# Optimization experiments

Measured on AMD Instinct MI355X. Metric: run time of the kernel, lower is better.

Reference implementation:

```python
import jax, jax.numpy as jnp
import numpy as np

DIM = 128
NUM_HEADS = 2
HEAD_DIM = DIM // NUM_HEADS
SCALE = HEAD_DIM ** -0.5
SR = 4
EPS_LN = 1e-5


def token2map(x, idx_token, H, W, H_init, W_init):
    """Scatter tokens x[B,N,Cc] into a [B,Cc,H,W] map via the init grid.
    Matches the sparse-COO branch of the torch token2map (N_init < N*H*W).
    """
    B, N, Cc = x.shape
    N_init = H_init * W_init
    # nearest-neighbor index of each init-grid cell in the HxW map
    rows = (jnp.arange(H_init) * H) // H_init          # floor(i * H / H_init)
    cols = (jnp.arange(W_init) * W) // W_init
    idx_hw = (rows[:, None] * W + cols[None, :]).reshape(-1)      # [N_init]
    flat = (idx_hw[None, :] + jnp.arange(B)[:, None] * (H * W)).reshape(-1)  # [B*N_init]
    # per-pixel count (A @ ones) + 1e-6, as in torch
    count = jax.ops.segment_sum(jnp.ones((B * N_init,), jnp.float32), flat,
                                num_segments=B * H * W) + 1e-6    # [B*H*W]
    gathered = jnp.take_along_axis(x, idx_token[..., None], axis=1)  # [B,N_init,Cc]
    out = jax.ops.segment_sum(gathered.reshape(B * N_init, Cc), flat,
                              num_segments=B * H * W)
    out = out / count[:, None]
    return out.reshape(B, H, W, Cc).transpose(0, 3, 1, 2)  # [B,Cc,H,W]


def setup_inputs() -> dict:
    key = jax.random.key(0)
    ks = jax.random.split(key, 12)
    B, Nq, Nkv, C = 8, 12544, 12544, DIM
    H, W, H_init, W_init = 112, 112, 224, 224
    inp = {
        'q_x': jax.random.normal(ks[0], (B, Nq, C), jnp.float32),
        'kv_x': jax.random.normal(ks[1], (B, Nkv, C), jnp.float32),
        'token_score': jax.random.normal(ks[2], (B, Nkv, 1), jnp.float32),
        'idx_token': jax.random.randint(ks[3], (B, H_init * W_init), 0, Nkv),
        'H': H, 'W': W, 'H_init': H_init, 'W_init': W_init,
        # learned params (qkv_bias=False)
        'q_w': jax.random.normal(ks[4], (C, C), jnp.float32) * 0.02,
        'kv_w': jax.random.normal(ks[5], (C, 2 * C), jnp.float32) * 0.02,
        'proj_w': jax.random.normal(ks[6], (C, C), jnp.float32) * 0.02,
        'proj_b': jnp.zeros((C,), jnp.float32),
        'sr_w': jax.random.normal(ks[7], (C, C, SR, SR), jnp.float32) * np.sqrt(2.0 / (SR * SR * C)),
        'sr_b': jnp.zeros((C,), jnp.float32),
        'norm_g': jnp.ones((C,), jnp.float32),
        'norm_b': jnp.zeros((C,), jnp.float32),
    }
    return inp


def reference(q_x, kv_x, token_score, q_w, kv_w, proj_w, proj_b, sr_w, sr_b,
              norm_g, norm_b, idx_token, H, W, H_init, W_init):
    B, Nq, C = q_x.shape
    # q projection -> [B, h, Nq, d]
    q = (q_x @ q_w).reshape(B, Nq, NUM_HEADS, HEAD_DIM).transpose(0, 2, 1, 3)

    # sr_ratio > 1 path: scatter kv tokens (with conf channel) to q's map
    tmp = jnp.concatenate([kv_x, token_score], axis=-1)          # [B,Nkv,C+1]
    tmp_map = token2map(tmp, idx_token, H, W, H_init, W_init)    # [B,C+1,H,W]
    kv_map = tmp_map[:, :C]                                      # [B,C,H,W]
    conf_map = tmp_map[:, C:]                                    # [B,1,H,W]

    # spatial reduction conv (kernel=stride=SR) + LayerNorm
    kv_r = jax.lax.conv_general_dilated(
        kv_map, sr_w, window_strides=(SR, SR), padding='VALID',
        dimension_numbers=('NCHW', 'OIHW', 'NCHW')) + sr_b[None, :, None, None]
    h, w = kv_r.shape[2], kv_r.shape[3]
    Ns = h * w
    kv_t = kv_r.reshape(B, C, Ns).transpose(0, 2, 1)             # [B,Ns,C]
    mu = jnp.mean(kv_t, axis=-1, keepdims=True)
    var = jnp.mean(jnp.square(kv_t - mu), axis=-1, keepdims=True)
    kv_t = (kv_t - mu) / jnp.sqrt(var + EPS_LN) * norm_g + norm_b

    # avg-pool conf to the reduced grid
    conf = conf_map.reshape(B, 1, h, SR, w, SR).mean(axis=(3, 5)).reshape(B, Ns)

    # kv projection -> k,v [B,h,Ns,d]
    kv_p = (kv_t @ kv_w).reshape(B, Ns, 2, NUM_HEADS, HEAD_DIM).transpose(2, 0, 3, 1, 4)
    k, v = kv_p[0], kv_p[1]

    attn = jnp.einsum('bhqd,bhkd->bhqk', q * SCALE, k) + conf[:, None, None, :]
    attn = jax.nn.softmax(attn, axis=-1)
    out = jnp.einsum('bhqk,bhkd->bhqd', attn, v).transpose(0, 2, 1, 3).reshape(B, Nq, C)
    return out @ proj_w + proj_b
```

## Files before the change

### kernel.cpp

```cpp
#include <hip/hip_runtime.h>
#include <hip/hip_bf16.h>


#define NBATCH 8
#define NQTOK  12544
#define NSP    832
#define LOG2E  1.4426950408889634f
#define QSCALE (0.125f * LOG2E)

typedef __attribute__((ext_vector_type(8))) short bf8;
typedef __attribute__((ext_vector_type(4))) float f4;
typedef __attribute__((ext_vector_type(4))) unsigned short u16x4;
typedef __attribute__((ext_vector_type(2))) unsigned int u32x2;

#define MFMA16(a, b, c) __builtin_amdgcn_mfma_f32_16x16x32_bf16((a), (b), (c), 0, 0, 0)

#if __has_builtin(__builtin_amdgcn_exp2f)
#define EXP2(x) __builtin_amdgcn_exp2f(x)
#else
#define EXP2(x) exp2f(x)
#endif

__device__ __forceinline__ unsigned short f2b(float x) {
  union { float f; unsigned u; } v; v.f = x;
  unsigned r = v.u + 0x7FFFu + ((v.u >> 16) & 1u);
  return (unsigned short)(r >> 16);
}

__device__ __forceinline__ unsigned pk2(float lo, float hi) {
  float2 t; t.x = lo; t.y = hi;
  __hip_bfloat162 bb = __float22bfloat162_rn(t);
  union { __hip_bfloat162 b; unsigned u; } v; v.b = bb;
  return v.u;
}

__device__ __forceinline__ bf8 rows2frag(const unsigned W0[2], const unsigned W1[2]) {
  u32x2 r0 = __builtin_amdgcn_permlane32_swap(W0[0], W1[0], false, false);
  u32x2 t02 = __builtin_amdgcn_permlane16_swap(r0.x, r0.y, false, false);
  u32x2 r1 = __builtin_amdgcn_permlane32_swap(W0[1], W1[1], false, false);
  u32x2 t13 = __builtin_amdgcn_permlane16_swap(r1.x, r1.y, false, false);
  union { unsigned u[4]; bf8 v; } pa;
  pa.u[0] = t02.x; pa.u[1] = t13.x; pa.u[2] = t02.y; pa.u[3] = t13.y;
  return pa.v;
}

__device__ __forceinline__ bf8 ldfrag(const unsigned short* t, int stride, int rbase, int kbase) {
  int lane = threadIdx.x & 63;
  return *(const bf8*)(t + (rbase + (lane & 15)) * stride + kbase + ((lane >> 4) << 3));
}

__global__ void k_token2map(const float* __restrict__ kv_x, const float* __restrict__ tsc,
                            const int* __restrict__ idxt,
                            unsigned short* __restrict__ kv_map, float* __restrict__ conf_map,
                            const float* __restrict__ qw, const float* __restrict__ kvw,
                            const float* __restrict__ pw, const float* __restrict__ srw,
                            unsigned short* __restrict__ qwt, unsigned short* __restrict__ kvwt,
                            unsigned short* __restrict__ pwt, unsigned short* __restrict__ srwt,
                            unsigned* __restrict__ kb, unsigned* __restrict__ vb,
                            float* __restrict__ conf) {
  int tid = threadIdx.x;
  int bid = blockIdx.x;
  if (bid >= 12544) {
    int t = (bid - 12544) * 256 + tid;
    int nt = 256 * 256;
    for (int i = t; i < 128 * 128; i += nt) {
      int k = i >> 7, n = i & 127;
      qwt[n * 128 + k] = f2b(qw[k * 128 + n] * QSCALE);
      pwt[n * 128 + k] = f2b(pw[k * 128 + n]);
    }
    for (int i = t; i < 128 * 256; i += nt) {
      int k = i >> 8, j = i & 255;
      kvwt[j * 128 + k] = f2b(kvw[k * 256 + j]);
    }
    for (int i = t; i < 128 * 2048; i += nt) {
      int o = i >> 11, kk = i & 2047;
      int p = kk >> 7, c = kk & 127;
      srwt[o * 2048 + kk] = f2b(srw[o * 2048 + c * 16 + p]);
    }
    const int nu = NBATCH * 2 * NSP * 64 / 2;
    for (int i = t; i < nu; i += nt) { kb[i] = 0u; vb[i] = 0u; }
    for (int i = t; i < NBATCH * NSP; i += nt) conf[i] = -1e30f;
    return;
  }
  int b = bid & 7, pos = bid >> 3;
  int hw = pos * 8 + (tid >> 5);
  int cell = b * 12544 + hw;
  int c0 = (tid & 31) << 2;
  int h = hw / 112, w = hw - h * 112;
  const int* it = idxt + b * 50176;
  int t0 = it[(2 * h) * 224 + 2 * w];
  int t1 = it[(2 * h) * 224 + 2 * w + 1];
  int t2 = it[(2 * h + 1) * 224 + 2 * w];
  int t3 = it[(2 * h + 1) * 224 + 2 * w + 1];
  const float* base = kv_x + (long)b * 12544 * 128 + c0;
  const float recip = 1.0f / (4.0f + 1e-6f);
  float4 a0 = *(const float4*)(base + (long)t0 * 128);
  float4 a1 = *(const float4*)(base + (long)t1 * 128);
  float4 a2 = *(const float4*)(base + (long)t2 * 128);
  float4 a3 = *(const float4*)(base + (long)t3 * 128);
  u16x4 o;
  o[0] = f2b((a0.x + a1.x + a2.x + a3.x) * recip);
  o[1] = f2b((a0.y + a1.y + a2.y + a3.y) * recip);
  o[2] = f2b((a0.z + a1.z + a2.z + a3.z) * recip);
  o[3] = f2b((a0.w + a1.w + a2.w + a3.w) * recip);
  *(u16x4*)(kv_map + (long)cell * 128 + c0) = o;
  if ((tid & 31) == 0) {
    const float* ts = tsc + b * 12544;
    conf_map[cell] = (ts[t0] + ts[t1] + ts[t2] + ts[t3]) * recip;
  }
}

__launch_bounds__(256)
__global__ void k_conv_ln_kv(const unsigned short* __restrict__ kv_map,
                             const unsigned short* __restrict__ srwt,
                             const float* __restrict__ srb, const float* __restrict__ ng,
                             const float* __restrict__ nb,
                             const unsigned short* __restrict__ kvwt,
                             unsigned short* __restrict__ kbuf,
                             unsigned short* __restrict__ vbuf,
                             const float* __restrict__ conf_map, float* __restrict__ conf) {
  __shared__ unsigned short At[64 * 136];
  __shared__ unsigned short Bt[128 * 136];
  const int tid = threadIdx.x;
  const int lane = tid & 63, w = tid >> 6;
  const int l15 = lane & 15, g = lane >> 4;
  const int r0 = blockIdx.x * 64;
  if (tid < 64) {
    int pos = r0 + tid;
    int bq = pos / 784, p2 = pos - bq * 784;
    int oh = p2 / 28, ow = p2 - oh * 28;
    float s = 0.f;
#pragma unroll
    for (int kh = 0; kh < 4; kh++)
#pragma unroll
      for (int kw = 0; kw < 4; kw++)
        s += conf_map[bq * 12544 + (4 * oh + kh) * 112 + 4 * ow + kw];
    conf[bq * NSP + p2] = s * (LOG2E / 16.0f);
  }
  const f4 fz = {0.f, 0.f, 0.f, 0.f};
  f4 acc[8];
#pragma unroll
  for (int i = 0; i < 8; i++) acc[i] = fz;

  for (int p = 0; p < 16; p++) {
#pragma unroll
    for (int j = 0; j < 4; j++) {
      int id = tid + 256 * j;
      int row = id >> 4, c0 = (id & 15) << 3;
      int rr = r0 + row;
      int bb = rr / 784, pos = rr - bb * 784;
      int oh = pos / 28, ow = pos - oh * 28;
      long src = ((long)(bb * 12544 + (4 * oh + (p >> 2)) * 112 + 4 * ow + (p & 3))) * 128 + c0;
      *(uint4*)(At + row * 136 + c0) = *(const uint4*)(kv_map + src);
    }
#pragma unroll
    for (int j = 0; j < 8; j++) {
      int id = tid + 256 * j;
      int row = id >> 4, c0 = (id & 15) << 3;
      *(uint4*)(Bt + row * 136 + c0) = *(const uint4*)(srwt + row * 2048 + p * 128 + c0);
    }
    __syncthreads();
#pragma unroll
    for (int ks = 0; ks < 4; ks++) {
      bf8 a = ldfrag(At, 136, 16 * w, 32 * ks);
#pragma unroll
      for (int nf = 0; nf < 8; nf++) {
        bf8 bb = ldfrag(Bt, 136, 16 * nf, 32 * ks);
        acc[nf] = MFMA16(a, bb, acc[nf]);
      }
    }
    __syncthreads();
  }
  float sum_[4] = {0.f, 0.f, 0.f, 0.f}, sq_[4] = {0.f, 0.f, 0.f, 0.f};
#pragma unroll
  for (int nf = 0; nf < 8; nf++) {
    float bias = srb[16 * nf + l15];
#pragma unroll
    for (int reg = 0; reg < 4; reg++) {
      float v = acc[nf][reg] + bias;
      acc[nf][reg] = v;
      sum_[reg] += v;
      sq_[reg] += v * v;
    }
  }
#pragma unroll
  for (int msk = 1; msk < 16; msk <<= 1)
#pragma unroll
    for (int reg = 0; reg < 4; reg++) {
      sum_[reg] += __shfl_xor(sum_[reg], msk, 64);
      sq_[reg] += __shfl_xor(sq_[reg], msk, 64);
    }
#pragma unroll
  for (int nf = 0; nf < 8; nf++) {
    float gc = ng[16 * nf + l15], bc = nb[16 * nf + l15];
#pragma unroll
    for (int reg = 0; reg < 4; reg++) {
      float mean = sum_[reg] * (1.0f / 128.0f);
      float var = sq_[reg] * (1.0f / 128.0f) - mean * mean;
      float v = (acc[nf][reg] - mean) * rsqrtf(var + 1e-5f) * gc + bc;
      At[(16 * w + 4 * g + reg) * 136 + 16 * nf + l15] = f2b(v);
    }
  }
  __syncthreads();
  f4 acc2[16];
#pragma unroll
  for (int i = 0; i < 16; i++) acc2[i] = fz;
#pragma unroll
  for (int ks = 0; ks < 4; ks++) {
    bf8 a = ldfrag(At, 136, 16 * w, 32 * ks);
#pragma unroll
    for (int nf = 0; nf < 16; nf++) {
      bf8 bb = *(const bf8*)(kvwt + (16 * nf + l15) * 128 + 32 * ks + (g << 3));
      acc2[nf] = MFMA16(a, bb, acc2[nf]);
    }
  }
#pragma unroll
  for (int nf = 0; nf < 16; nf++)
#pragma unroll
    for (int reg = 0; reg < 4; reg++) {
      int r = r0 + 16 * w + 4 * g + reg;
      int b = r / 784, ns = r - b * 784;
      int j = 16 * nf + l15;
      int sel = j >> 7, hh = (j >> 6) & 1, d = j & 63;
      unsigned short val = f2b(acc2[nf][reg]);
      if (sel == 0) kbuf[((long)(b * 2 + hh) * NSP + ns) * 64 + d] = val;
      else          vbuf[((long)(b * 2 + hh) * 64 + d) * NSP + ns] = val;
    }
}

__launch_bounds__(256)
__global__ void k_q(const float* __restrict__ q_x, const unsigned short* __restrict__ qwt,
                    unsigned short* __restrict__ qbuf) {
  __shared__ unsigned short At[64 * 136];
  __shared__ unsigned short Bt[128 * 136];
  const int tid = threadIdx.x;
  const int lane = tid & 63, w = tid >> 6;
  const int l15 = lane & 15, g = lane >> 4;
  const int bid = blockIdx.x;
  const int r0 = (bid & 7) * NQTOK + (bid >> 3) * 64;
#pragma unroll
  for (int j = 0; j < 8; j++) {
    int id = tid + 256 * j;
    int row = id >> 5, c0 = (id & 31) << 2;
    float4 v = *(const float4*)(q_x + (long)(r0 + row) * 128 + c0);
    u16x4 o;
    o[0] = f2b(v.x); o[1] = f2b(v.y); o[2] = f2b(v.z); o[3] = f2b(v.w);
    *(u16x4*)(At + row * 136 + c0) = o;
  }
#pragma unroll
  for (int j = 0; j < 8; j++) {
    int id = tid + 256 * j;
    int row = id >> 4, c0 = (id & 15) << 3;
    *(uint4*)(Bt + row * 136 + c0) = *(const uint4*)(qwt + (long)row * 128 + c0);
  }
  __syncthreads();
  const f4 fz = {0.f, 0.f, 0.f, 0.f};
  f4 acc[8];
#pragma unroll
  for (int i = 0; i < 8; i++) acc[i] = fz;
#pragma unroll
  for (int ks = 0; ks < 4; ks++) {
    bf8 a = ldfrag(At, 136, 16 * w, 32 * ks);
#pragma unroll
    for (int nf = 0; nf < 8; nf++) {
      bf8 bb = ldfrag(Bt, 136, 16 * nf, 32 * ks);
      acc[nf] = MFMA16(a, bb, acc[nf]);
    }
  }
#pragma unroll
  for (int nf = 0; nf < 8; nf++)
#pragma unroll
    for (int reg = 0; reg < 4; reg++) {
      int r = r0 + 16 * w + 4 * g + reg;
      int b = r / NQTOK, n = r - b * NQTOK;
      int j = 16 * nf + l15;
      int hh = j >> 6, d = j & 63;
      qbuf[((long)(b * 2 + hh) * NQTOK + n) * 64 + d] = f2b(acc[nf][reg]);
    }
}

__launch_bounds__(256, 3)
__global__ void k_attn(const unsigned short* __restrict__ qbuf,
                       const unsigned short* __restrict__ kbuf,
                       const unsigned short* __restrict__ vbuf,
                       const float* __restrict__ conf,
                       unsigned short* __restrict__ attbuf) {
  __shared__ unsigned short Kt[2][64 * 72];
  __shared__ unsigned short Vt[2][64 * 72];
  const int tid = threadIdx.x;
  const int lane = tid & 63, w = tid >> 6;
  const int l15 = lane & 15, g = lane >> 4;
  const int bid = blockIdx.x;
  const int xcd = bid & 7, idx = bid >> 3;
  const int sub = idx / 98;
  const int xb = idx - sub * 98;
  const int bhid = xcd * 2 + sub;
  const int b = bhid >> 1, h = bhid & 1;
  const int bh = b * 2 + h;
  const int q0 = xb * 128 + 32 * w;

  const unsigned short* qsrc = qbuf + ((long)bh * NQTOK + q0) * 64;
  bf8 qf[2][2];
#pragma unroll
  for (int mr = 0; mr < 2; mr++)
#pragma unroll
    for (int ks = 0; ks < 2; ks++)
      qf[mr][ks] = *(const bf8*)(qsrc + (16 * mr + l15) * 64 + 32 * ks + (g << 3));

  const int srow = tid >> 2;
  const int scol = (tid & 3) << 4;
  const unsigned short* kg = kbuf + (long)bh * NSP * 64 + srow * 64 + scol;
  const unsigned short* vg = vbuf + (long)bh * 64 * NSP + (long)srow * NSP + scol;
  unsigned short* klds = &Kt[0][0] + srow * 72 + scol;
  unsigned short* vlds = &Vt[0][0] + srow * 72 + scol;

  uint4 kr0, kr1, vr0, vr1;
#define ISSUE(T)                                                   \
  do {                                                             \
    const unsigned short* kp_ = kg + (long)(T) * 4096;             \
    const unsigned short* vp_ = vg + (T) * 64;                     \
    kr0 = *(const uint4*)(kp_);                                    \
    kr1 = *(const uint4*)(kp_ + 8);                                \
    vr0 = *(const uint4*)(vp_);                                    \
    vr1 = *(const uint4*)(vp_ + 8);                                \
  } while (0)
#define STWRITE(BUF)                                               \
  do {                                                             \
    unsigned short* kd_ = klds + (BUF) * 4608;                     \
    unsigned short* vd_ = vlds + (BUF) * 4608;                     \
    *(uint4*)kd_ = kr0;  *(uint4*)(kd_ + 8) = kr1;                 \
    *(uint4*)vd_ = vr0;  *(uint4*)(vd_ + 8) = vr1;                 \
  } while (0)

  ISSUE(0);
  STWRITE(0);
  ISSUE(1);
  __syncthreads();

  const f4 fz = {0.f, 0.f, 0.f, 0.f};
  f4 ao[2][4], aol[2];
#pragma unroll
  for (int mr = 0; mr < 2; mr++) {
    aol[mr] = fz;
#pragma unroll
    for (int i = 0; i < 4; i++) ao[mr][i] = fz;
  }
  const short on = (short)0x3F80;
  const bf8 onesf = {on, on, on, on, on, on, on, on};
  const float* confb = conf + b * NSP;

#pragma unroll 2
  for (int t = 0; t < 13; t++) {
    const int cur = t & 1;
    const unsigned short* KtB = &Kt[cur][0];
    const unsigned short* VtB = &Vt[cur][0];
    bf8 kf[4][2];
#pragma unroll
    for (int mf = 0; mf < 4; mf++)
#pragma unroll
      for (int ks = 0; ks < 2; ks++)
        kf[mf][ks] = ldfrag(KtB, 72, 16 * mf, 32 * ks);
    bf8 vf[4][2];
#pragma unroll
    for (int nfd = 0; nfd < 4; nfd++)
#pragma unroll
      for (int ks = 0; ks < 2; ks++)
        vf[nfd][ks] = ldfrag(VtB, 72, 16 * nfd, 32 * ks);
    f4 cvi[4];
#pragma unroll
    for (int mf = 0; mf < 4; mf++) {
      float4 cv = *(const float4*)(confb + t * 64 + 16 * mf + 4 * g);
      cvi[mf][0] = cv.x; cvi[mf][1] = cv.y; cvi[mf][2] = cv.z; cvi[mf][3] = cv.w;
    }
#pragma unroll
    for (int mr = 0; mr < 2; mr++) {
      f4 s_[4];
#pragma unroll
      for (int mf = 0; mf < 4; mf++) s_[mf] = cvi[mf];
#pragma unroll
      for (int ks = 0; ks < 2; ks++)
#pragma unroll
        for (int mf = 0; mf < 4; mf++)
          s_[mf] = MFMA16(kf[mf][ks], qf[mr][ks], s_[mf]);
      unsigned W[4][2];
#pragma unroll
      for (int mf = 0; mf < 4; mf++) {
        float p0 = EXP2(s_[mf][0]);
        float p1 = EXP2(s_[mf][1]);
        float p2 = EXP2(s_[mf][2]);
        float p3 = EXP2(s_[mf][3]);
        W[mf][0] = pk2(p0, p1);
        W[mf][1] = pk2(p2, p3);
      }
#pragma unroll
      for (int ks = 0; ks < 2; ks++) {
        bf8 pa = rows2frag(W[2 * ks], W[2 * ks + 1]);
        aol[mr] = MFMA16(pa, onesf, aol[mr]);
#pragma unroll
        for (int nfd = 0; nfd < 4; nfd++)
          ao[mr][nfd] = MFMA16(pa, vf[nfd][ks], ao[mr][nfd]);
      }
    }
    if (t < 12) STWRITE(cur ^ 1);
    if (t < 11) ISSUE(t + 2);
    __syncthreads();
  }
#undef ISSUE
#undef STWRITE
#pragma unroll
  for (int mr = 0; mr < 2; mr++) {
    float inv[4];
#pragma unroll
    for (int reg = 0; reg < 4; reg++) inv[reg] = 1.0f / aol[mr][reg];
#pragma unroll
    for (int nfd = 0; nfd < 4; nfd++)
#pragma unroll
      for (int reg = 0; reg < 4; reg++) {
        int n = q0 + 16 * mr + 4 * g + reg;
        int col = h * 64 + 16 * nfd + l15;
        attbuf[((long)b * NQTOK + n) * 128 + col] = f2b(ao[mr][nfd][reg] * inv[reg]);
      }
  }
}

__launch_bounds__(256)
__global__ void k_proj(const unsigned short* __restrict__ attbuf,
                       const unsigned short* __restrict__ pwt,
                       const float* __restrict__ pb, float* __restrict__ out) {
  __shared__ unsigned short At[64 * 136];
  __shared__ unsigned short Bt[128 * 136];
  const int tid = threadIdx.x;
  const int lane = tid & 63, w = tid >> 6;
  const int l15 = lane & 15, g = lane >> 4;
  const int bid = blockIdx.x;
  const int r0 = (bid & 7) * NQTOK + (bid >> 3) * 64;
#pragma unroll
  for (int j = 0; j < 4; j++) {
    int id = tid + 256 * j;
    int row = id >> 4, c0 = (id & 15) << 3;
    *(uint4*)(At + row * 136 + c0) = *(const uint4*)(attbuf + (long)(r0 + row) * 128 + c0);
  }
#pragma unroll
  for (int j = 0; j < 8; j++) {
    int id = tid + 256 * j;
    int row = id >> 4, c0 = (id & 15) << 3;
    *(uint4*)(Bt + row * 136 + c0) = *(const uint4*)(pwt + (long)row * 128 + c0);
  }
  __syncthreads();
  const f4 fz = {0.f, 0.f, 0.f, 0.f};
  f4 acc[8];
#pragma unroll
  for (int i = 0; i < 8; i++) acc[i] = fz;
#pragma unroll
  for (int ks = 0; ks < 4; ks++) {
    bf8 a = ldfrag(At, 136, 16 * w, 32 * ks);
#pragma unroll
    for (int nf = 0; nf < 8; nf++) {
      bf8 bb = ldfrag(Bt, 136, 16 * nf, 32 * ks);
      acc[nf] = MFMA16(a, bb, acc[nf]);
    }
  }
#pragma unroll
  for (int nf = 0; nf < 8; nf++) {
    float bias = pb[16 * nf + l15];
#pragma unroll
    for (int reg = 0; reg < 4; reg++) {
      int r = r0 + 16 * w + 4 * g + reg;
      out[(long)r * 128 + 16 * nf + l15] = acc[nf][reg] + bias;
    }
  }
}

extern "C" void kernel_launch(void* const* d_in, const int* in_sizes, int n_in,
                              void* d_out, int out_size, void* d_ws, size_t ws_size,
                              hipStream_t stream) {
  const float* q_x  = (const float*)d_in[0];
  const float* kv_x = (const float*)d_in[1];
  const float* tsc  = (const float*)d_in[2];
  const int*   idxt = (const int*)d_in[3];
  const float* q_w  = (const float*)d_in[8];
  const float* kv_w = (const float*)d_in[9];
  const float* pw   = (const float*)d_in[10];
  const float* pb   = (const float*)d_in[11];
  const float* srw  = (const float*)d_in[12];
  const float* srb  = (const float*)d_in[13];
  const float* ng   = (const float*)d_in[14];
  const float* nb   = (const float*)d_in[15];
  float* outp = (float*)d_out;

  char* ws = (char*)d_ws;
  size_t off = 0;
  auto take = [&](size_t bytes) {
    char* p = ws + off;
    off += (bytes + 255) & ~(size_t)255;
    return p;
  };
  unsigned short* qwt   = (unsigned short*)take(128 * 128 * 2);
  unsigned short* pwt   = (unsigned short*)take(128 * 128 * 2);
  unsigned short* kvwt  = (unsigned short*)take(256 * 128 * 2);
  unsigned short* srwt  = (unsigned short*)take(128 * 2048 * 2);
  unsigned short* kvmap = (unsigned short*)take((size_t)NBATCH * 12544 * 128 * 2);
  float* conf_map       = (float*)take((size_t)NBATCH * 12544 * 4);
  unsigned short* kbuf  = (unsigned short*)take((size_t)NBATCH * 2 * NSP * 64 * 2);
  unsigned short* vbuf  = (unsigned short*)take((size_t)NBATCH * 2 * NSP * 64 * 2);
  float* conf           = (float*)take((size_t)NBATCH * NSP * 4);
  unsigned short* qbuf  = (unsigned short*)take((size_t)NBATCH * 2 * NQTOK * 64 * 2);
  unsigned short* attbuf = kvmap;

  k_token2map<<<12800, 256, 0, stream>>>(kv_x, tsc, idxt, kvmap, conf_map,
                                         q_w, kv_w, pw, srw, qwt, kvwt, pwt, srwt,
                                         (unsigned*)kbuf, (unsigned*)vbuf, conf);
  k_conv_ln_kv<<<98, 256, 0, stream>>>(kvmap, srwt, srb, ng, nb, kvwt, kbuf, vbuf,
                                       conf_map, conf);
  k_q<<<1568, 256, 0, stream>>>(q_x, qwt, qbuf);
  k_attn<<<1568, 256, 0, stream>>>(qbuf, kbuf, vbuf, conf, attbuf);
  k_proj<<<1568, 256, 0, stream>>>(attbuf, pwt, pb, outp);
}
```

Measured before the change: 160.2 us.

## Split weight setup kernel, fuse Q projection into token2map, read B operand from global

Weight conversion and buffer clearing move into their own small kernel. The Q projection GEMM is merged into the token2map launch as extra blocks, so the two independent workloads run concurrently and one launch is removed. The conv, Q and proj GEMMs now read their weight B-fragments straight from global or L2 instead of staging them in shared memory, which cuts LDS footprint and a load phase but adds uncoalesced global reads. The attention score MFMA chain is also reordered slightly.

Measured after the change: 248.5 us. +55.1%, slower.

```diff
diff --git a/kernel.cpp b/kernel.cpp
--- a/kernel.cpp
+++ b/kernel.cpp
@@ -49,37 +49,80 @@
   return *(const bf8*)(t + (rbase + (lane & 15)) * stride + kbase + ((lane >> 4) << 3));
 }
 
-__global__ void k_token2map(const float* __restrict__ kv_x, const float* __restrict__ tsc,
-                            const int* __restrict__ idxt,
-                            unsigned short* __restrict__ kv_map, float* __restrict__ conf_map,
-                            const float* __restrict__ qw, const float* __restrict__ kvw,
-                            const float* __restrict__ pw, const float* __restrict__ srw,
-                            unsigned short* __restrict__ qwt, unsigned short* __restrict__ kvwt,
-                            unsigned short* __restrict__ pwt, unsigned short* __restrict__ srwt,
-                            unsigned* __restrict__ kb, unsigned* __restrict__ vb,
-                            float* __restrict__ conf) {
-  int tid = threadIdx.x;
-  int bid = blockIdx.x;
+__global__ void k_setup(const float* __restrict__ qw, const float* __restrict__ kvw,
+                        const float* __restrict__ pw, const float* __restrict__ srw,
+                        unsigned short* __restrict__ qwt, unsigned short* __restrict__ kvwt,
+                        unsigned short* __restrict__ pwt, unsigned short* __restrict__ srwt,
+                        unsigned* __restrict__ kb, unsigned* __restrict__ vb,
+                        float* __restrict__ conf) {
+  int tid = blockIdx.x * 256 + threadIdx.x;
+  int nt = gridDim.x * 256;
+  for (int i = tid; i < 128 * 128; i += nt) {
+    int k = i >> 7, n = i & 127;
+    qwt[n * 128 + k] = f2b(qw[k * 128 + n] * QSCALE);
+    pwt[n * 128 + k] = f2b(pw[k * 128 + n]);
+  }
+  for (int i = tid; i < 128 * 256; i += nt) {
+    int k = i >> 8, j = i & 255;
+    kvwt[j * 128 + k] = f2b(kvw[k * 256 + j]);
+  }
+  for (int i = tid; i < 128 * 2048; i += nt) {
+    int o = i >> 11, kk = i & 2047;
+    int p = kk >> 7, c = kk & 127;
+    srwt[o * 2048 + kk] = f2b(srw[o * 2048 + c * 16 + p]);
+  }
+  const int nu = NBATCH * 2 * NSP * 64 / 2;
+  for (int i = tid; i < nu; i += nt) { kb[i] = 0u; vb[i] = 0u; }
+  for (int i = tid; i < NBATCH * NSP; i += nt) conf[i] = -1e30f;
+}
+
+__launch_bounds__(256)
+__global__ void k_tokq(const float* __restrict__ kv_x, const float* __restrict__ tsc,
+                       const int* __restrict__ idxt,
+                       unsigned short* __restrict__ kv_map, float* __restrict__ conf_map,
+                       const float* __restrict__ q_x, const unsigned short* __restrict__ qwt,
+                       unsigned short* __restrict__ qbuf) {
+  __shared__ unsigned short At[64 * 136];
+  const int tid = threadIdx.x;
+  const int bid = blockIdx.x;
   if (bid >= 12544) {
-    int t = (bid - 12544) * 256 + tid;
-    int nt = 256 * 256;
-    for (int i = t; i < 128 * 128; i += nt) {
-      int k = i >> 7, n = i & 127;
-      qwt[n * 128 + k] = f2b(qw[k * 128 + n] * QSCALE);
-      pwt[n * 128 + k] = f2b(pw[k * 128 + n]);
-    }
-    for (int i = t; i < 128 * 256; i += nt) {
-      int k = i >> 8, j = i & 255;
-      kvwt[j * 128 + k] = f2b(kvw[k * 256 + j]);
-    }
-    for (int i = t; i < 128 * 2048; i += nt) {
-      int o = i >> 11, kk = i & 2047;
-      int p = kk >> 7, c = kk & 127;
-      srwt[o * 2048 + kk] = f2b(srw[o * 2048 + c * 16 + p]);
-    }
-    const int nu = NBATCH * 2 * NSP * 64 / 2;
-    for (int i = t; i < nu; i += nt) { kb[i] = 0u; vb[i] = 0u; }
-    for (int i = t; i < NBATCH * NSP; i += nt) conf[i] = -1e30f;
+    const int qb = bid - 12544;
+    const int lane = tid & 63, w = tid >> 6;
+    const int l15 = lane & 15, g = lane >> 4;
+    const int r0 = (qb & 7) * NQTOK + (qb >> 3) * 64;
+#pragma unroll
+    for (int j = 0; j < 8; j++) {
+      int id = tid + 256 * j;
+      int row = id >> 5, c0 = (id & 31) << 2;
+      float4 v = *(const float4*)(q_x + (long)(r0 + row) * 128 + c0);
+      u16x4 o;
+      o[0] = f2b(v.x); o[1] = f2b(v.y); o[2] = f2b(v.z); o[3] = f2b(v.w);
+      *(u16x4*)(At + row * 136 + c0) = o;
+    }
+    __syncthreads();
+    const f4 fz = {0.f, 0.f, 0.f, 0.f};
+    f4 acc[8];
+#pragma unroll
+    for (int i = 0; i < 8; i++) acc[i] = fz;
+#pragma unroll
+    for (int ks = 0; ks < 4; ks++) {
+      bf8 a = ldfrag(At, 136, 16 * w, 32 * ks);
+#pragma unroll
+      for (int nf = 0; nf < 8; nf++) {
+        bf8 bb = *(const bf8*)(qwt + (16 * nf + l15) * 128 + 32 * ks + (g << 3));
+        acc[nf] = MFMA16(a, bb, acc[nf]);
+      }
+    }
+#pragma unroll
+    for (int nf = 0; nf < 8; nf++)
+#pragma unroll
+      for (int reg = 0; reg < 4; reg++) {
+        int r = r0 + 16 * w + 4 * g + reg;
+        int b = r / NQTOK, n = r - b * NQTOK;
+        int j = 16 * nf + l15;
+        int hh = j >> 6, d = j & 63;
+        qbuf[((long)(b * 2 + hh) * NQTOK + n) * 64 + d] = f2b(acc[nf][reg]);
+      }
     return;
   }
   int b = bid & 7, pos = bid >> 3;
@@ -120,7 +163,6 @@
                              unsigned short* __restrict__ vbuf,
                              const float* __restrict__ conf_map, float* __restrict__ conf) {
   __shared__ unsigned short At[64 * 136];
-  __shared__ unsigned short Bt[128 * 136];
   const int tid = threadIdx.x;
   const int lane = tid & 63, w = tid >> 6;
   const int l15 = lane & 15, g = lane >> 4;
@@ -153,19 +195,13 @@
       long src = ((long)(bb * 12544 + (4 * oh + (p >> 2)) * 112 + 4 * ow + (p & 3))) * 128 + c0;
       *(uint4*)(At + row * 136 + c0) = *(const uint4*)(kv_map + src);
     }
-#pragma unroll
-    for (int j = 0; j < 8; j++) {
-      int id = tid + 256 * j;
-      int row = id >> 4, c0 = (id & 15) << 3;
-      *(uint4*)(Bt + row * 136 + c0) = *(const uint4*)(srwt + row * 2048 + p * 128 + c0);
-    }
     __syncthreads();
 #pragma unroll
     for (int ks = 0; ks < 4; ks++) {
       bf8 a = ldfrag(At, 136, 16 * w, 32 * ks);
 #pragma unroll
       for (int nf = 0; nf < 8; nf++) {
-        bf8 bb = ldfrag(Bt, 136, 16 * nf, 32 * ks);
+        bf8 bb = *(const bf8*)(srwt + (16 * nf + l15) * 2048 + p * 128 + 32 * ks + (g << 3));
         acc[nf] = MFMA16(a, bb, acc[nf]);
       }
     }
@@ -225,57 +261,6 @@
       unsigned short val = f2b(acc2[nf][reg]);
       if (sel == 0) kbuf[((long)(b * 2 + hh) * NSP + ns) * 64 + d] = val;
       else          vbuf[((long)(b * 2 + hh) * 64 + d) * NSP + ns] = val;
-    }
-}
-
-__launch_bounds__(256)
-__global__ void k_q(const float* __restrict__ q_x, const unsigned short* __restrict__ qwt,
-                    unsigned short* __restrict__ qbuf) {
-  __shared__ unsigned short At[64 * 136];
-  __shared__ unsigned short Bt[128 * 136];
-  const int tid = threadIdx.x;
-  const int lane = tid & 63, w = tid >> 6;
-  const int l15 = lane & 15, g = lane >> 4;
-  const int bid = blockIdx.x;
-  const int r0 = (bid & 7) * NQTOK + (bid >> 3) * 64;
-#pragma unroll
-  for (int j = 0; j < 8; j++) {
-    int id = tid + 256 * j;
-    int row = id >> 5, c0 = (id & 31) << 2;
-    float4 v = *(const float4*)(q_x + (long)(r0 + row) * 128 + c0);
-    u16x4 o;
-    o[0] = f2b(v.x); o[1] = f2b(v.y); o[2] = f2b(v.z); o[3] = f2b(v.w);
-    *(u16x4*)(At + row * 136 + c0) = o;
-  }
-#pragma unroll
-  for (int j = 0; j < 8; j++) {
-    int id = tid + 256 * j;
-    int row = id >> 4, c0 = (id & 15) << 3;
-    *(uint4*)(Bt + row * 136 + c0) = *(const uint4*)(qwt + (long)row * 128 + c0);
-  }
-  __syncthreads();
-  const f4 fz = {0.f, 0.f, 0.f, 0.f};
-  f4 acc[8];
-#pragma unroll
-  for (int i = 0; i < 8; i++) acc[i] = fz;
-#pragma unroll
-  for (int ks = 0; ks < 4; ks++) {
-    bf8 a = ldfrag(At, 136, 16 * w, 32 * ks);
-#pragma unroll
-    for (int nf = 0; nf < 8; nf++) {
-      bf8 bb = ldfrag(Bt, 136, 16 * nf, 32 * ks);
-      acc[nf] = MFMA16(a, bb, acc[nf]);
-    }
-  }
-#pragma unroll
-  for (int nf = 0; nf < 8; nf++)
-#pragma unroll
-    for (int reg = 0; reg < 4; reg++) {
-      int r = r0 + 16 * w + 4 * g + reg;
-      int b = r / NQTOK, n = r - b * NQTOK;
-      int j = 16 * nf + l15;
-      int hh = j >> 6, d = j & 63;
-      qbuf[((long)(b * 2 + hh) * NQTOK + n) * 64 + d] = f2b(acc[nf][reg]);
     }
 }
 
@@ -376,12 +361,11 @@
     for (int mr = 0; mr < 2; mr++) {
       f4 s_[4];
 #pragma unroll
-      for (int mf = 0; mf < 4; mf++) s_[mf] = cvi[mf];
-#pragma unroll
-      for (int ks = 0; ks < 2; ks++)
-#pragma unroll
-        for (int mf = 0; mf < 4; mf++)
-          s_[mf] = MFMA16(kf[mf][ks], qf[mr][ks], s_[mf]);
+      for (int mf = 0; mf < 4; mf++)
+        s_[mf] = MFMA16(kf[mf][0], qf[mr][0], cvi[mf]);
+#pragma unroll
+      for (int mf = 0; mf < 4; mf++)
+        s_[mf] = MFMA16(kf[mf][1], qf[mr][1], s_[mf]);
       unsigned W[4][2];
 #pragma unroll
       for (int mf = 0; mf < 4; mf++) {
@@ -428,7 +412,6 @@
                        const unsigned short* __restrict__ pwt,
                        const float* __restrict__ pb, float* __restrict__ out) {
   __shared__ unsigned short At[64 * 136];
-  __shared__ unsigned short Bt[128 * 136];
   const int tid = threadIdx.x;
   const int lane = tid & 63, w = tid >> 6;
   const int l15 = lane & 15, g = lane >> 4;
@@ -440,12 +423,6 @@
     int row = id >> 4, c0 = (id & 15) << 3;
     *(uint4*)(At + row * 136 + c0) = *(const uint4*)(attbuf + (long)(r0 + row) * 128 + c0);
   }
-#pragma unroll
-  for (int j = 0; j < 8; j++) {
-    int id = tid + 256 * j;
-    int row = id >> 4, c0 = (id & 15) << 3;
-    *(uint4*)(Bt + row * 136 + c0) = *(const uint4*)(pwt + (long)row * 128 + c0);
-  }
   __syncthreads();
   const f4 fz = {0.f, 0.f, 0.f, 0.f};
   f4 acc[8];
@@ -456,7 +433,7 @@
     bf8 a = ldfrag(At, 136, 16 * w, 32 * ks);
 #pragma unroll
     for (int nf = 0; nf < 8; nf++) {
-      bf8 bb = ldfrag(Bt, 136, 16 * nf, 32 * ks);
+      bf8 bb = *(const bf8*)(pwt + (16 * nf + l15) * 128 + 32 * ks + (g << 3));
       acc[nf] = MFMA16(a, bb, acc[nf]);
     }
   }
@@ -507,12 +484,12 @@
   unsigned short* qbuf  = (unsigned short*)take((size_t)NBATCH * 2 * NQTOK * 64 * 2);
   unsigned short* attbuf = kvmap;
 
-  k_token2map<<<12800, 256, 0, stream>>>(kv_x, tsc, idxt, kvmap, conf_map,
-                                         q_w, kv_w, pw, srw, qwt, kvwt, pwt, srwt,
-                                         (unsigned*)kbuf, (unsigned*)vbuf, conf);
+  k_setup<<<256, 256, 0, stream>>>(q_w, kv_w, pw, srw, qwt, kvwt, pwt, srwt,
+                                   (unsigned*)kbuf, (unsigned*)vbuf, conf);
+  k_tokq<<<14112, 256, 0, stream>>>(kv_x, tsc, idxt, kvmap, conf_map,
+                                    q_x, qwt, qbuf);
   k_conv_ln_kv<<<98, 256, 0, stream>>>(kvmap, srwt, srb, ng, nb, kvwt, kbuf, vbuf,
                                        conf_map, conf);
-  k_q<<<1568, 256, 0, stream>>>(q_x, qwt, qbuf);
   k_attn<<<1568, 256, 0, stream>>>(qbuf, kbuf, vbuf, conf, attbuf);
   k_proj<<<1568, 256, 0, stream>>>(attbuf, pwt, pb, outp);
 }
```
